# Optimization experiments

Hardware: AMD Instinct MI355X
Metric: run time of the kernel (lower is better)

The kernel has to match this reference:

```python
import jax, jax.numpy as jnp
import numpy as np


def setup_inputs() -> dict:
    key = jax.random.key(0)
    ks = jax.random.split(key, 8)
    B, T, I, H, O = 4096, 2048, 4, 20, 4
    s_ih = 1.0 / np.sqrt(H)
    return {
        "x": jax.random.normal(ks[0], (B, T, I), dtype=jnp.float32),
        "h0": jax.random.normal(ks[1], (B, H), dtype=jnp.float32),
        "W_ih": jax.random.uniform(ks[2], (H, I), jnp.float32, -s_ih, s_ih),
        "W_hh": jax.random.uniform(ks[3], (H, H), jnp.float32, -s_ih, s_ih),
        "b_ih": jax.random.uniform(ks[4], (H,), jnp.float32, -s_ih, s_ih),
        "b_hh": jax.random.uniform(ks[5], (H,), jnp.float32, -s_ih, s_ih),
        "fc_w": jax.random.uniform(ks[6], (O, H), jnp.float32, -s_ih, s_ih),
        "fc_b": jax.random.uniform(ks[7], (O,), jnp.float32, -s_ih, s_ih),
    }


def reference(x, h0, W_ih, W_hh, b_ih, b_hh, fc_w, fc_b):
    # x: [B, T, I] batch_first; vanilla tanh RNN recurrence.
    # Precompute the input projection for all timesteps in one GEMM.
    xi = jnp.einsum("bti,hi->tbh", x, W_ih) + b_ih + b_hh  # [T, B, H]

    def step(h, xt):
        h = jnp.tanh(xt + h @ W_hh.T)  # [B, H]
        return h, None

    h_last, _ = jax.lax.scan(step, h0, xi)
    # Module takes last timestep only, then Linear(H -> 4).
    return h_last @ fc_w.T + fc_b  # [B, 4]
```

## Files before the change

### kernel.cpp

```cpp
#include <hip/hip_runtime.h>
#include <cstddef>


typedef float f32x2 __attribute__((ext_vector_type(2)));
typedef float f32x4 __attribute__((ext_vector_type(4)));

constexpr int Tn   = 2048;
constexpr int Hn   = 20;
constexpr int EPB  = 16;
constexpr int SB   = 16;
constexpr int NBLK = Tn / SB;

__global__ __launch_bounds__(256, 1) void rnn_fwd(
    const float* __restrict__ x,
    const float* __restrict__ h0,
    const float* __restrict__ W_ih,
    const float* __restrict__ W_hh,
    const float* __restrict__ b_ih,
    const float* __restrict__ b_hh,
    const float* __restrict__ fc_w,
    const float* __restrict__ fc_b,
    float* __restrict__ out)
{
    __shared__ __align__(16) f32x4 xlds[2][EPB][SB + 1];
    __shared__ float hsh[EPB][24];

    const int tid  = threadIdx.x;
    const int j    = tid & 15;
    const int e    = tid >> 4;
    const int b    = blockIdx.x * EPB + e;
    const int uB   = 16 + (j & 3);
    const int lane = tid & 63;

    const int iQ  = (lane & ~3) << 2;
    const int iID = lane << 2;
    const int i12 = (((lane & ~15) | ((lane - 12) & 15))) << 2;
    const int i13 = (((lane & ~15) | ((lane - 13) & 15))) << 2;
    const int i14 = (((lane & ~15) | ((lane - 14) & 15))) << 2;
    const int i15 = (((lane & ~15) | ((lane - 15) & 15))) << 2;

    const float S = 2.88539008177792681472f;

    f32x2 w2[16];
#pragma unroll
    for (int r = 0; r < 16; ++r) {
        const int k = (j - r) & 15;
        w2[r] = f32x2{S * W_hh[j * Hn + k], S * W_hh[uB * Hn + k]};
    }
    f32x2 wq2[4], xiw[4];
#pragma unroll
    for (int c = 0; c < 4; ++c) {
        wq2[c] = f32x2{S * W_hh[j * Hn + 16 + c], S * W_hh[uB * Hn + 16 + c]};
        xiw[c] = f32x2{S * W_ih[j * 4 + c],       S * W_ih[uB * 4 + c]};
    }
    f32x2 bias2 = f32x2{S * (b_ih[j] + b_hh[j]), S * (b_ih[uB] + b_hh[uB])};

    float rA = 0.5f * (1.0f - h0[b * Hn + j]);
    float rB = 0.5f * (1.0f - h0[b * Hn + uB]);
    float hA, hB;

    const f32x4* __restrict__ xp =
        reinterpret_cast<const f32x4*>(x) + (size_t)b * Tn;

#define DPPM " row_mask:0xf bank_mask:0xf\n\t"
#define PKB  " op_sel:[0,0,0] op_sel_hi:[1,0,1]\n\t"
#define CLB  "v42","v43","v44","v45","v46","v47","v48","v49","v50","v51",     \
             "v52","v53","v54","v55","v56","v57","v58","v59","v60","v61",     \
             "v62","v63","v64","v65"

#define STEP_MAC() do {                                                       \
    asm volatile(                                                             \
  "v_fma_f32 %[hB], %[rB], -2.0, 1.0\n\t"                                     \
  "v_fma_f32 %[hA], %[rA], -2.0, 1.0\n\t"                                     \
  "ds_bpermute_b32 v42, %[iQ], %[hB]\n\t"                                     \
  "ds_bpermute_b32 v44, %[iQ], %[hB] offset:4\n\t"                            \
  "ds_bpermute_b32 v46, %[iQ], %[hB] offset:8\n\t"                            \
  "ds_bpermute_b32 v48, %[iQ], %[hB] offset:12\n\t"                           \
  "ds_bpermute_b32 v50, %[i12], %[hA]\n\t"                                    \
  "ds_bpermute_b32 v52, %[i13], %[hA]\n\t"                                    \
  "ds_bpermute_b32 v54, %[i14], %[hA]\n\t"                                    \
  "ds_bpermute_b32 v56, %[i15], %[hA]\n\t"                                    \
  "ds_bpermute_b32 v58, %[iID], %[hA]\n\t"                                    \
  "v_mov_b32_dpp v60, %[hA] row_ror:1"  DPPM                                  \
  "v_mov_b32_dpp v62, %[hA] row_ror:2"  DPPM                                  \
  "v_pk_fma_f32 %[Q], %[w1], v[60:61], %[Q]" PKB                              \
  "v_mov_b32_dpp v64, %[hA] row_ror:3"  DPPM                                  \
  "v_pk_fma_f32 %[R], %[w2], v[62:63], %[R]" PKB                              \
  "v_mov_b32_dpp v60, %[hA] row_ror:4"  DPPM                                  \
  "v_pk_fma_f32 %[Sc], %[w3], v[64:65], %[Sc]" PKB                            \
  "v_mov_b32_dpp v62, %[hA] row_ror:5"  DPPM                                  \
  "v_pk_fma_f32 %[P], %[w4], v[60:61], %[P]" PKB                              \
  "v_mov_b32_dpp v64, %[hA] row_ror:6"  DPPM                                  \
  "v_pk_fma_f32 %[Q], %[w5], v[62:63], %[Q]" PKB                              \
  "v_mov_b32_dpp v60, %[hA] row_ror:7"  DPPM                                  \
  "v_pk_fma_f32 %[R], %[w6], v[64:65], %[R]" PKB                              \
  "v_mov_b32_dpp v62, %[hA] row_ror:8"  DPPM                                  \
  "v_pk_fma_f32 %[Sc], %[w7], v[60:61], %[Sc]" PKB                            \
  "v_mov_b32_dpp v64, %[hA] row_ror:9"  DPPM                                  \
  "v_pk_fma_f32 %[P], %[w8], v[62:63], %[P]" PKB                              \
  "v_mov_b32_dpp v60, %[hA] row_ror:10" DPPM                                  \
  "v_pk_fma_f32 %[Q], %[w9], v[64:65], %[Q]" PKB                              \
  "v_mov_b32_dpp v62, %[hA] row_ror:11" DPPM                                  \
  "v_pk_fma_f32 %[R], %[w10], v[60:61], %[R]" PKB                             \
  "v_pk_fma_f32 %[Sc], %[w11], v[62:63], %[Sc]"                               \
  " op_sel:[0,0,0] op_sel_hi:[1,0,1]"                                         \
  : [hA] "=&v"(hA), [hB] "=&v"(hB),                                           \
    [P] "+v"(xiP), [Q] "+v"(xiQ), [R] "+v"(xiR), [Sc] "+v"(xiS)               \
  : [rA] "v"(rA), [rB] "v"(rB),                                               \
    [w1] "v"(w2[1]), [w2] "v"(w2[2]),  [w3] "v"(w2[3]),  [w4] "v"(w2[4]),     \
    [w5] "v"(w2[5]), [w6] "v"(w2[6]),  [w7] "v"(w2[7]),  [w8] "v"(w2[8]),     \
    [w9] "v"(w2[9]), [w10] "v"(w2[10]),[w11] "v"(w2[11]),                     \
    [iQ] "v"(iQ), [iID] "v"(iID),                                             \
    [i12] "v"(i12), [i13] "v"(i13), [i14] "v"(i14), [i15] "v"(i15)            \
  : CLB);                                                                     \
} while (0)

#define STEP_TAIL(XV) do {                                                    \
    f32x2 xa_ = __builtin_shufflevector((XV), (XV), 0, 1);                    \
    f32x2 xb_ = __builtin_shufflevector((XV), (XV), 2, 3);                    \
    asm volatile(                                                             \
  "s_waitcnt lgkmcnt(0)\n\t"                                                  \
  "v_pk_fma_f32 %[P],  %[w0],  v[58:59], %[P]" PKB          \
  "v_pk_fma_f32 %[Q],  %[w13], v[52:53], %[Q]" PKB                  \
  "v_pk_fma_f32 %[R],  %[w14], v[54:55], %[R]" PKB                  \
  "v_pk_fma_f32 %[Sc], %[w15], v[56:57], %[Sc]" PKB                 \
  "v_pk_fma_f32 %[P],  %[w12], v[50:51], %[P]" PKB                  \
  "v_pk_fma_f32 %[Q],  %[q1w], v[44:45], %[Q]" PKB                \
  "v_pk_fma_f32 %[R],  %[q2w], v[46:47], %[R]" PKB                \
  "v_pk_fma_f32 %[Sc], %[q3w], v[48:49], %[Sc]" PKB               \
  "v_pk_fma_f32 %[P],  %[q0w], v[42:43], %[P]" PKB                \
  "v_pk_add_f32 v[60:61], %[P], %[Q]\n\t"                                     \
  "v_pk_fma_f32 %[P], %[x0], %[xa], %[b2]" PKB                                \
  "v_pk_add_f32 v[62:63], %[R], %[Sc]\n\t"                                    \
  "v_pk_mul_f32 %[Q], %[x1], %[xa] op_sel:[0,1] op_sel_hi:[1,1]\n\t"          \
  "v_pk_mul_f32 %[R], %[x2], %[xb] op_sel:[0,0] op_sel_hi:[1,0]\n\t"          \
  "v_pk_add_f32 v[60:61], v[60:61], v[62:63]\n\t"                             \
  "v_pk_mul_f32 %[Sc], %[x3], %[xb] op_sel:[0,1] op_sel_hi:[1,1]\n\t"         \
  "v_exp_f32 v64, v61\n\t"                                                    \
  "v_exp_f32 v65, v60\n\t"                                                    \
  "v_add_f32 v64, 1.0, v64\n\t"                                               \
  "v_add_f32 v65, 1.0, v65\n\t"                                               \
  "v_rcp_f32 %[rB], v64\n\t"                                                  \
  "v_rcp_f32 %[rA], v65"                                                      \
  : [rA] "=&v"(rA), [rB] "=&v"(rB),                                           \
    [P] "+v"(xiP), [Q] "+v"(xiQ), [R] "+v"(xiR), [Sc] "+v"(xiS)               \
  : [w0] "v"(w2[0]), [w12] "v"(w2[12]), [w13] "v"(w2[13]),                    \
    [w14] "v"(w2[14]), [w15] "v"(w2[15]),                                     \
    [q0w] "v"(wq2[0]), [q1w] "v"(wq2[1]), [q2w] "v"(wq2[2]), [q3w] "v"(wq2[3]),\
    [xa] "v"(xa_), [xb] "v"(xb_),                                             \
    [x0] "v"(xiw[0]), [x1] "v"(xiw[1]), [x2] "v"(xiw[2]), [x3] "v"(xiw[3]),   \
    [b2] "v"(bias2)                                                           \
  : CLB);                                                                     \
} while (0)

#define STEP(XV) do { STEP_MAC(); STEP_TAIL(XV); } while (0)

    xlds[0][e][j] = xp[j];
    f32x4 x0v = xp[0];
    f32x2 xiP = f32x2{__builtin_fmaf(x0v[0], xiw[0][0], bias2[0]),
                      __builtin_fmaf(x0v[0], xiw[0][1], bias2[1])};
    f32x2 xiQ = f32x2{x0v[1] * xiw[1][0], x0v[1] * xiw[1][1]};
    f32x2 xiR = f32x2{x0v[2] * xiw[2][0], x0v[2] * xiw[2][1]};
    f32x2 xiS = f32x2{x0v[3] * xiw[3][0], x0v[3] * xiw[3][1]};
    f32x4 q0 = xlds[0][e][1];
    f32x4 q1 = xlds[0][e][2];
    f32x4 q2 = xlds[0][e][3];

    int cur = 0;
#pragma unroll 1
    for (int k = 0; k < NBLK; ++k) {
        const int kn = (k + 1 < NBLK) ? (k + 1) : (NBLK - 1);
        f32x4 xr = xp[kn * SB + j];
        const int nxt = cur ^ 1;
#pragma unroll
        for (int s = 0; s < SB - 4; ++s) {
            f32x4 xv = q0; q0 = q1; q1 = q2;
            q2 = xlds[cur][e][s + 4];
            STEP(xv);
        }
        xlds[nxt][e][j] = xr;
        { f32x4 xv = q0; q0 = q1; q1 = q2; q2 = xlds[nxt][e][0]; STEP(xv); }
        { f32x4 xv = q0; q0 = q1; q1 = q2; q2 = xlds[nxt][e][1]; STEP(xv); }
        { f32x4 xv = q0; q0 = q1; q1 = q2; q2 = xlds[nxt][e][2]; STEP(xv); }
        { f32x4 xv = q0; q0 = q1; q1 = q2; q2 = xlds[nxt][e][3]; STEP(xv); }
        cur = nxt;
    }
#undef STEP
#undef STEP_MAC
#undef STEP_TAIL
#undef PKB
#undef DPPM
#undef CLB

    const float hAf = __builtin_fmaf(-2.0f, rA, 1.0f);
    const float hBf = __builtin_fmaf(-2.0f, rB, 1.0f);

    hsh[e][j] = hAf;
    if (j < 4) hsh[e][16 + j] = hBf;
    if (j < 4) {
        float o = fc_b[j];
#pragma unroll
        for (int kk = 0; kk < Hn; ++kk)
            o = __builtin_fmaf(hsh[e][kk], fc_w[j * Hn + kk], o);
        out[b * 4 + j] = o;
    }
}

extern "C" void kernel_launch(void* const* d_in, const int* in_sizes, int n_in,
                              void* d_out, int out_size, void* d_ws, size_t ws_size,
                              hipStream_t stream) {
    const float* x    = (const float*)d_in[0];
    const float* h0   = (const float*)d_in[1];
    const float* W_ih = (const float*)d_in[2];
    const float* W_hh = (const float*)d_in[3];
    const float* b_ih = (const float*)d_in[4];
    const float* b_hh = (const float*)d_in[5];
    const float* fc_w = (const float*)d_in[6];
    const float* fc_b = (const float*)d_in[7];
    float* out = (float*)d_out;

    rnn_fwd<<<dim3(256), dim3(256), 0, stream>>>(x, h0, W_ih, W_hh, b_ih, b_hh,
                                                 fc_w, fc_b, out);
}
```

Baseline: 448.5 us.

## Replace bpermute broadcasts with quad DPP and use two accumulator chains

The per-step recurrence now gathers the four tail hidden units (indices 16-19) with quad_perm DPP moves instead of four ds_bpermute ops. The self term comes straight from the register rather than through an identity bpermute. The packed accumulators drop from four to two (P, Q), and the tail weights are re-indexed to match the rotated quad order. This removes LDS-path permutes and a reduction add from the serial critical path, at the cost of longer dependent FMA chains on two accumulators.

Measured after the change: 425.0 us. -5.2%, faster.

```diff
diff --git a/kernel.cpp b/kernel.cpp
--- a/kernel.cpp
+++ b/kernel.cpp
@@ -32,8 +32,6 @@
     const int uB   = 16 + (j & 3);
     const int lane = tid & 63;
 
-    const int iQ  = (lane & ~3) << 2;
-    const int iID = lane << 2;
     const int i12 = (((lane & ~15) | ((lane - 12) & 15))) << 2;
     const int i13 = (((lane & ~15) | ((lane - 13) & 15))) << 2;
     const int i14 = (((lane & ~15) | ((lane - 14) & 15))) << 2;
@@ -47,72 +45,74 @@
         const int k = (j - r) & 15;
         w2[r] = f32x2{S * W_hh[j * Hn + k], S * W_hh[uB * Hn + k]};
     }
-    f32x2 wq2[4], xiw[4];
+    f32x2 wqr[4], xiw[4];
 #pragma unroll
     for (int c = 0; c < 4; ++c) {
-        wq2[c] = f32x2{S * W_hh[j * Hn + 16 + c], S * W_hh[uB * Hn + 16 + c]};
-        xiw[c] = f32x2{S * W_ih[j * 4 + c],       S * W_ih[uB * 4 + c]};
+        const int qc = 16 + ((j + c) & 3);
+        wqr[c] = f32x2{S * W_hh[j * Hn + qc], S * W_hh[uB * Hn + qc]};
+        xiw[c] = f32x2{S * W_ih[j * 4 + c],  S * W_ih[uB * 4 + c]};
     }
     f32x2 bias2 = f32x2{S * (b_ih[j] + b_hh[j]), S * (b_ih[uB] + b_hh[uB])};
 
     float rA = 0.5f * (1.0f - h0[b * Hn + j]);
     float rB = 0.5f * (1.0f - h0[b * Hn + uB]);
-    float hA, hB;
 
     const f32x4* __restrict__ xp =
         reinterpret_cast<const f32x4*>(x) + (size_t)b * Tn;
 
 #define DPPM " row_mask:0xf bank_mask:0xf\n\t"
 #define PKB  " op_sel:[0,0,0] op_sel_hi:[1,0,1]\n\t"
-#define CLB  "v42","v43","v44","v45","v46","v47","v48","v49","v50","v51",     \
-             "v52","v53","v54","v55","v56","v57","v58","v59","v60","v61",     \
-             "v62","v63","v64","v65"
+#define CLB  "v40","v41","v42","v43","v44","v45","v46","v47","v48","v49",     \
+             "v50","v51","v52","v53","v54","v55","v56","v57","v58","v59",     \
+             "v60","v61","v62","v63"
 
 #define STEP_MAC() do {                                                       \
     asm volatile(                                                             \
-  "v_fma_f32 %[hB], %[rB], -2.0, 1.0\n\t"                                     \
-  "v_fma_f32 %[hA], %[rA], -2.0, 1.0\n\t"                                     \
-  "ds_bpermute_b32 v42, %[iQ], %[hB]\n\t"                                     \
-  "ds_bpermute_b32 v44, %[iQ], %[hB] offset:4\n\t"                            \
-  "ds_bpermute_b32 v46, %[iQ], %[hB] offset:8\n\t"                            \
-  "ds_bpermute_b32 v48, %[iQ], %[hB] offset:12\n\t"                           \
-  "ds_bpermute_b32 v50, %[i12], %[hA]\n\t"                                    \
-  "ds_bpermute_b32 v52, %[i13], %[hA]\n\t"                                    \
-  "ds_bpermute_b32 v54, %[i14], %[hA]\n\t"                                    \
-  "ds_bpermute_b32 v56, %[i15], %[hA]\n\t"                                    \
-  "ds_bpermute_b32 v58, %[iID], %[hA]\n\t"                                    \
-  "v_mov_b32_dpp v60, %[hA] row_ror:1"  DPPM                                  \
-  "v_mov_b32_dpp v62, %[hA] row_ror:2"  DPPM                                  \
-  "v_pk_fma_f32 %[Q], %[w1], v[60:61], %[Q]" PKB                              \
-  "v_mov_b32_dpp v64, %[hA] row_ror:3"  DPPM                                  \
-  "v_pk_fma_f32 %[R], %[w2], v[62:63], %[R]" PKB                              \
-  "v_mov_b32_dpp v60, %[hA] row_ror:4"  DPPM                                  \
-  "v_pk_fma_f32 %[Sc], %[w3], v[64:65], %[Sc]" PKB                            \
-  "v_mov_b32_dpp v62, %[hA] row_ror:5"  DPPM                                  \
-  "v_pk_fma_f32 %[P], %[w4], v[60:61], %[P]" PKB                              \
-  "v_mov_b32_dpp v64, %[hA] row_ror:6"  DPPM                                  \
-  "v_pk_fma_f32 %[Q], %[w5], v[62:63], %[Q]" PKB                              \
-  "v_mov_b32_dpp v60, %[hA] row_ror:7"  DPPM                                  \
-  "v_pk_fma_f32 %[R], %[w6], v[64:65], %[R]" PKB                              \
-  "v_mov_b32_dpp v62, %[hA] row_ror:8"  DPPM                                  \
-  "v_pk_fma_f32 %[Sc], %[w7], v[60:61], %[Sc]" PKB                            \
-  "v_mov_b32_dpp v64, %[hA] row_ror:9"  DPPM                                  \
-  "v_pk_fma_f32 %[P], %[w8], v[62:63], %[P]" PKB                              \
-  "v_mov_b32_dpp v60, %[hA] row_ror:10" DPPM                                  \
-  "v_pk_fma_f32 %[Q], %[w9], v[64:65], %[Q]" PKB                              \
-  "v_mov_b32_dpp v62, %[hA] row_ror:11" DPPM                                  \
-  "v_pk_fma_f32 %[R], %[w10], v[60:61], %[R]" PKB                             \
-  "v_pk_fma_f32 %[Sc], %[w11], v[62:63], %[Sc]"                               \
+  "v_fma_f32 v44, %[rB], -2.0, 1.0\n\t"                 \
+  "v_fma_f32 v40, %[rA], -2.0, 1.0\n\t"                 \
+  "ds_bpermute_b32 v50, %[i12], v40\n\t"                                      \
+  "ds_bpermute_b32 v52, %[i13], v40\n\t"                                      \
+  "ds_bpermute_b32 v54, %[i14], v40\n\t"                                      \
+  "ds_bpermute_b32 v56, %[i15], v40\n\t"                                      \
+  "v_pk_fma_f32 %[P], %[w0], v[40:41], %[P]" PKB              \
+  "v_mov_b32_dpp v42, v44 quad_perm:[1,2,3,0]" DPPM                           \
+  "v_pk_fma_f32 %[Q], %[c0], v[44:45], %[Q]" PKB             \
+  "v_mov_b32_dpp v46, v44 quad_perm:[2,3,0,1]" DPPM                           \
+  "v_pk_fma_f32 %[P], %[c1], v[42:43], %[P]" PKB                              \
+  "v_mov_b32_dpp v48, v44 quad_perm:[3,0,1,2]" DPPM                           \
+  "v_pk_fma_f32 %[Q], %[c2], v[46:47], %[Q]" PKB                              \
+  "v_mov_b32_dpp v42, v40 row_ror:1"  DPPM                                    \
+  "v_pk_fma_f32 %[P], %[c3], v[48:49], %[P]" PKB                              \
+  "v_mov_b32_dpp v46, v40 row_ror:2"  DPPM                                    \
+  "v_pk_fma_f32 %[Q], %[w1], v[42:43], %[Q]" PKB                              \
+  "v_mov_b32_dpp v48, v40 row_ror:3"  DPPM                                    \
+  "v_pk_fma_f32 %[P], %[w2], v[46:47], %[P]" PKB                              \
+  "v_mov_b32_dpp v42, v40 row_ror:4"  DPPM                                    \
+  "v_pk_fma_f32 %[Q], %[w3], v[48:49], %[Q]" PKB                              \
+  "v_mov_b32_dpp v46, v40 row_ror:5"  DPPM                                    \
+  "v_pk_fma_f32 %[P], %[w4], v[42:43], %[P]" PKB                              \
+  "v_mov_b32_dpp v48, v40 row_ror:6"  DPPM                                    \
+  "v_pk_fma_f32 %[Q], %[w5], v[46:47], %[Q]" PKB                              \
+  "v_mov_b32_dpp v42, v40 row_ror:7"  DPPM                                    \
+  "v_pk_fma_f32 %[P], %[w6], v[48:49], %[P]" PKB                              \
+  "v_mov_b32_dpp v46, v40 row_ror:8"  DPPM                                    \
+  "v_pk_fma_f32 %[Q], %[w7], v[42:43], %[Q]" PKB                              \
+  "v_mov_b32_dpp v48, v40 row_ror:9"  DPPM                                    \
+  "v_pk_fma_f32 %[P], %[w8], v[46:47], %[P]" PKB                              \
+  "v_mov_b32_dpp v42, v40 row_ror:10" DPPM                                    \
+  "v_pk_fma_f32 %[Q], %[w9], v[48:49], %[Q]" PKB                              \
+  "v_mov_b32_dpp v46, v40 row_ror:11" DPPM                                    \
+  "v_pk_fma_f32 %[P], %[w10], v[42:43], %[P]" PKB                             \
+  "v_pk_fma_f32 %[Q], %[w11], v[46:47], %[Q]"                                 \
   " op_sel:[0,0,0] op_sel_hi:[1,0,1]"                                         \
-  : [hA] "=&v"(hA), [hB] "=&v"(hB),                                           \
-    [P] "+v"(xiP), [Q] "+v"(xiQ), [R] "+v"(xiR), [Sc] "+v"(xiS)               \
+  : [P] "+v"(xiP), [Q] "+v"(xiQ)                                              \
   : [rA] "v"(rA), [rB] "v"(rB),                                               \
-    [w1] "v"(w2[1]), [w2] "v"(w2[2]),  [w3] "v"(w2[3]),  [w4] "v"(w2[4]),     \
-    [w5] "v"(w2[5]), [w6] "v"(w2[6]),  [w7] "v"(w2[7]),  [w8] "v"(w2[8]),     \
-    [w9] "v"(w2[9]), [w10] "v"(w2[10]),[w11] "v"(w2[11]),                     \
-    [iQ] "v"(iQ), [iID] "v"(iID),                                             \
+    [w0] "v"(w2[0]), [w1] "v"(w2[1]),  [w2] "v"(w2[2]),  [w3] "v"(w2[3]),     \
+    [w4] "v"(w2[4]), [w5] "v"(w2[5]),  [w6] "v"(w2[6]),  [w7] "v"(w2[7]),     \
+    [w8] "v"(w2[8]), [w9] "v"(w2[9]),  [w10] "v"(w2[10]),[w11] "v"(w2[11]),   \
+    [c0] "v"(wqr[0]), [c1] "v"(wqr[1]), [c2] "v"(wqr[2]), [c3] "v"(wqr[3]),   \
     [i12] "v"(i12), [i13] "v"(i13), [i14] "v"(i14), [i15] "v"(i15)            \
-  : CLB);                                                                     \
+  : CLB, "memory");                                                           \
 } while (0)
 
 #define STEP_TAIL(XV) do {                                                    \
@@ -120,48 +120,41 @@
     f32x2 xb_ = __builtin_shufflevector((XV), (XV), 2, 3);                    \
     asm volatile(                                                             \
   "s_waitcnt lgkmcnt(0)\n\t"                                                  \
-  "v_pk_fma_f32 %[P],  %[w0],  v[58:59], %[P]" PKB          \
-  "v_pk_fma_f32 %[Q],  %[w13], v[52:53], %[Q]" PKB                  \
-  "v_pk_fma_f32 %[R],  %[w14], v[54:55], %[R]" PKB                  \
-  "v_pk_fma_f32 %[Sc], %[w15], v[56:57], %[Sc]" PKB                 \
-  "v_pk_fma_f32 %[P],  %[w12], v[50:51], %[P]" PKB                  \
-  "v_pk_fma_f32 %[Q],  %[q1w], v[44:45], %[Q]" PKB                \
-  "v_pk_fma_f32 %[R],  %[q2w], v[46:47], %[R]" PKB                \
-  "v_pk_fma_f32 %[Sc], %[q3w], v[48:49], %[Sc]" PKB               \
-  "v_pk_fma_f32 %[P],  %[q0w], v[42:43], %[P]" PKB                \
-  "v_pk_add_f32 v[60:61], %[P], %[Q]\n\t"                                     \
+  "v_pk_fma_f32 %[P], %[w12], v[50:51], %[P]" PKB                   \
+  "v_pk_fma_f32 %[Q], %[w13], v[52:53], %[Q]" PKB                   \
+  "v_pk_fma_f32 %[P], %[w14], v[54:55], %[P]" PKB                   \
+  "v_pk_fma_f32 %[Q], %[w15], v[56:57], %[Q]" PKB                   \
+  "v_pk_add_f32 v[58:59], %[P], %[Q]\n\t"                                     \
   "v_pk_fma_f32 %[P], %[x0], %[xa], %[b2]" PKB                                \
-  "v_pk_add_f32 v[62:63], %[R], %[Sc]\n\t"                                    \
   "v_pk_mul_f32 %[Q], %[x1], %[xa] op_sel:[0,1] op_sel_hi:[1,1]\n\t"          \
-  "v_pk_mul_f32 %[R], %[x2], %[xb] op_sel:[0,0] op_sel_hi:[1,0]\n\t"          \
-  "v_pk_add_f32 v[60:61], v[60:61], v[62:63]\n\t"                             \
-  "v_pk_mul_f32 %[Sc], %[x3], %[xb] op_sel:[0,1] op_sel_hi:[1,1]\n\t"         \
-  "v_exp_f32 v64, v61\n\t"                                                    \
-  "v_exp_f32 v65, v60\n\t"                                                    \
-  "v_add_f32 v64, 1.0, v64\n\t"                                               \
-  "v_add_f32 v65, 1.0, v65\n\t"                                               \
-  "v_rcp_f32 %[rB], v64\n\t"                                                  \
-  "v_rcp_f32 %[rA], v65"                                                      \
+  "v_exp_f32 v60, v59\n\t"                                                    \
+  "v_pk_fma_f32 %[P], %[x2], %[xb], %[P]" PKB                                 \
+  "v_exp_f32 v61, v58\n\t"                                                    \
+  "v_pk_fma_f32 %[Q], %[x3], %[xb], %[Q] op_sel:[0,1,0] op_sel_hi:[1,1,1]\n\t"\
+  "v_add_f32 v60, 1.0, v60\n\t"                                               \
+  "v_add_f32 v61, 1.0, v61\n\t"                                               \
+  "v_rcp_f32 %[rB], v60\n\t"                                                  \
+  "v_rcp_f32 %[rA], v61"                                                      \
   : [rA] "=&v"(rA), [rB] "=&v"(rB),                                           \
-    [P] "+v"(xiP), [Q] "+v"(xiQ), [R] "+v"(xiR), [Sc] "+v"(xiS)               \
-  : [w0] "v"(w2[0]), [w12] "v"(w2[12]), [w13] "v"(w2[13]),                    \
-    [w14] "v"(w2[14]), [w15] "v"(w2[15]),                                     \
-    [q0w] "v"(wq2[0]), [q1w] "v"(wq2[1]), [q2w] "v"(wq2[2]), [q3w] "v"(wq2[3]),\
+    [P] "+v"(xiP), [Q] "+v"(xiQ)                                              \
+  : [w12] "v"(w2[12]), [w13] "v"(w2[13]), [w14] "v"(w2[14]), [w15] "v"(w2[15]),\
     [xa] "v"(xa_), [xb] "v"(xb_),                                             \
     [x0] "v"(xiw[0]), [x1] "v"(xiw[1]), [x2] "v"(xiw[2]), [x3] "v"(xiw[3]),   \
     [b2] "v"(bias2)                                                           \
-  : CLB);                                                                     \
+  : CLB, "memory");                                                           \
 } while (0)
 
 #define STEP(XV) do { STEP_MAC(); STEP_TAIL(XV); } while (0)
 
     xlds[0][e][j] = xp[j];
     f32x4 x0v = xp[0];
-    f32x2 xiP = f32x2{__builtin_fmaf(x0v[0], xiw[0][0], bias2[0]),
-                      __builtin_fmaf(x0v[0], xiw[0][1], bias2[1])};
-    f32x2 xiQ = f32x2{x0v[1] * xiw[1][0], x0v[1] * xiw[1][1]};
-    f32x2 xiR = f32x2{x0v[2] * xiw[2][0], x0v[2] * xiw[2][1]};
-    f32x2 xiS = f32x2{x0v[3] * xiw[3][0], x0v[3] * xiw[3][1]};
+    f32x2 xiP, xiQ;
+    xiP[0] = __builtin_fmaf(x0v[2], xiw[2][0],
+             __builtin_fmaf(x0v[0], xiw[0][0], bias2[0]));
+    xiP[1] = __builtin_fmaf(x0v[2], xiw[2][1],
+             __builtin_fmaf(x0v[0], xiw[0][1], bias2[1]));
+    xiQ[0] = __builtin_fmaf(x0v[3], xiw[3][0], x0v[1] * xiw[1][0]);
+    xiQ[1] = __builtin_fmaf(x0v[3], xiw[3][1], x0v[1] * xiw[1][1]);
     f32x4 q0 = xlds[0][e][1];
     f32x4 q1 = xlds[0][e][2];
     f32x4 q2 = xlds[0][e][3];
```
